# Kernel optimization log

Measured on AMD Instinct MI355X. Metric: run time of the kernel, lower is better.

Reference implementation:

```python
import jax, jax.numpy as jnp
import numpy as np

DIM = 512
HEADS = 8
EPS = 1e-5


def layer_norm(x, g, b):
    mu = jnp.mean(x, axis=-1, keepdims=True)
    var = jnp.mean(jnp.square(x - mu), axis=-1, keepdims=True)
    return (x - mu) * jax.lax.rsqrt(var + EPS) * g + b


def setup_inputs() -> dict:
    key = jax.random.key(0)
    ks = jax.random.split(key, 8)
    d = DIM
    s = 0.02
    return {
        "x": jax.random.normal(ks[0], (2, d, 64, 64), jnp.float32),
        "ln1_g": jnp.ones((d,), jnp.float32),
        "ln1_b": jnp.zeros((d,), jnp.float32),
        "w_qkv": jax.random.normal(ks[1], (d, 3 * d), jnp.float32) * s,
        "b_qkv": jnp.zeros((3 * d,), jnp.float32),
        "w_proj": jax.random.normal(ks[2], (d, d), jnp.float32) * s,
        "b_proj": jnp.zeros((d,), jnp.float32),
        "ln2_g": jnp.ones((d,), jnp.float32),
        "ln2_b": jnp.zeros((d,), jnp.float32),
        "w_ffn1": jax.random.normal(ks[3], (d, 4 * d), jnp.float32) * s,
        "b_ffn1": jnp.zeros((4 * d,), jnp.float32),
        "w_ffn2": jax.random.normal(ks[4], (4 * d, d), jnp.float32) * s,
        "b_ffn2": jnp.zeros((d,), jnp.float32),
    }


def reference(x, ln1_g, ln1_b, w_qkv, b_qkv, w_proj, b_proj,
              ln2_g, ln2_b, w_ffn1, b_ffn1, w_ffn2, b_ffn2):
    B, C, H, W = x.shape
    hd = C // HEADS
    x_in = x
    t = x.reshape(B, C, H * W).transpose(0, 2, 1)  # [B, N, C]
    h = layer_norm(t, ln1_g, ln1_b)
    qkv = h @ w_qkv + b_qkv  # [B, N, 3C]
    q, k, v = jnp.split(qkv, 3, axis=-1)
    def to_heads(a):
        return a.reshape(B, -1, HEADS, hd).transpose(0, 2, 1, 3)  # [B, h, N, hd]
    q, k, v = to_heads(q), to_heads(k), to_heads(v)
    # NOTE: module scales by 1/sqrt(C), not 1/sqrt(head_dim)
    attn = jnp.einsum('bhqd,bhkd->bhqk', q, k) / jnp.sqrt(jnp.float32(C))
    attn = jax.nn.softmax(attn, axis=-1)
    out = jnp.einsum('bhqk,bhkd->bhqd', attn, v)
    out = out.transpose(0, 2, 1, 3).reshape(B, -1, C)
    out = out @ w_proj + b_proj
    t = t + out
    h2 = layer_norm(t, ln2_g, ln2_b)
    ffn = jax.nn.relu(h2 @ w_ffn1 + b_ffn1) @ w_ffn2 + b_ffn2
    t = t + ffn
    y = t.transpose(0, 2, 1).reshape(B, C, H, W)
    return y + x_in
```

## Files before the change

kernel.cpp:

```cpp
#include <hip/hip_runtime.h>
#include <hip/hip_bf16.h>

typedef __bf16 bf16;
typedef __bf16 bf16x8 __attribute__((ext_vector_type(8)));
typedef __bf16 bf16x4 __attribute__((ext_vector_type(4)));
typedef __bf16 bf16x2 __attribute__((ext_vector_type(2)));
typedef float f32x4 __attribute__((ext_vector_type(4)));
typedef int int4v __attribute__((ext_vector_type(4)));
typedef int int2v __attribute__((ext_vector_type(2)));

#define DEV static __device__ __forceinline__

DEV void gload16(const void* g, void* l) {
    __builtin_amdgcn_global_load_lds(
        (const __attribute__((address_space(1))) void*)g,
        (__attribute__((address_space(3))) void*)l, 16, 0, 0);
}

DEV f32x4 mfma16(bf16x8 a, bf16x8 b, f32x4 c) {
    return __builtin_amdgcn_mfma_f32_16x16x32_bf16(a, b, c, 0, 0, 0);
}

DEV int cvtpk(float lo, float hi) {
    int r;
    asm("v_cvt_pk_bf16_f32 %0, %1, %2" : "=v"(r) : "v"(lo), "v"(hi));
    return r;
}

DEV float rexp2(float x) {
    float r;
    asm("v_exp_f32 %0, %1" : "=v"(r) : "v"(x));
    return r;
}

template <bool HASPO>
__global__ __launch_bounds__(512, 2)
void k_tln(const float* __restrict__ x, const bf16* __restrict__ po,
           const float* __restrict__ gg, const float* __restrict__ bb,
           bf16* __restrict__ h) {
    __shared__ char sm[HASPO ? 69632 : 35840];
    bf16* big = (bf16*)sm;
    float* red = (float*)(sm + 33536);
    float* mures = (float*)(sm + 35584);
    bf16* pob = (bf16*)(sm + 35840);

    int t = threadIdx.x;
    int bid = blockIdx.x;
    int nt = bid & 127, b = bid >> 7;
    int n0 = nt * 32;

    if (HASPO) {
        int rr = t >> 4, cs16 = t & 15;
        const bf16* ps = po + (size_t)(b * 4096 + n0 + rr) * 512 + cs16 * 32;
#pragma unroll
        for (int j = 0; j < 4; j++)
            *(bf16x8*)&pob[rr * 524 + cs16 * 32 + j * 8] =
                *(const bf16x8*)(ps + j * 8);
        __syncthreads();
    }

    int n = t & 31, cg = t >> 5;
    const float* xp = x + (size_t)b * 512 * 4096 +
                      (size_t)(cg * 32) * 4096 + n0 + n;
    float s = 0.f, ss = 0.f;
#pragma unroll
    for (int i = 0; i < 32; i++) {
        float v = xp[(size_t)i * 4096];
        if (HASPO) v += (float)pob[n * 524 + cg * 32 + i];
        s += v;
        ss += v * v;
        big[n * 524 + cg * 32 + i] = (bf16)v;
    }
    s += __shfl_xor(s, 32);
    ss += __shfl_xor(ss, 32);
    int w = t >> 6, l = t & 63;
    if (l < 32) {
        red[(w * 32 + n) * 2] = s;
        red[(w * 32 + n) * 2 + 1] = ss;
    }
    __syncthreads();
    if (t < 32) {
        float ts = 0.f, tss = 0.f;
#pragma unroll
        for (int ww = 0; ww < 8; ww++) {
            ts += red[(ww * 32 + t) * 2];
            tss += red[(ww * 32 + t) * 2 + 1];
        }
        float mu = ts * (1.f / 512.f);
        float var = tss * (1.f / 512.f) - mu * mu;
        mures[t * 2] = mu;
        mures[t * 2 + 1] = rsqrtf(var + 1e-5f);
    }
    __syncthreads();

    int nw = t >> 4, cs = t & 15;
    float mu = mures[nw * 2], rs = mures[nw * 2 + 1];
    bf16* hd = h + (size_t)(b * 4096 + n0 + nw) * 512;
#pragma unroll
    for (int j = 0; j < 4; j++) {
        int c = cs * 8 + j * 128;
        bf16x8 vv = *(const bf16x8*)&big[nw * 524 + c];
        f32x4 g0v = *(const f32x4*)(gg + c);
        f32x4 g1v = *(const f32x4*)(gg + c + 4);
        f32x4 b0v = *(const f32x4*)(bb + c);
        f32x4 b1v = *(const f32x4*)(bb + c + 4);
        bf16x8 o;
#pragma unroll
        for (int k = 0; k < 4; k++) {
            o[k] = (bf16)(((float)vv[k] - mu) * rs * g0v[k] + b0v[k]);
            o[k + 4] = (bf16)(((float)vv[k + 4] - mu) * rs * g1v[k] + b1v[k]);
        }
        *(bf16x8*)(hd + c) = o;
    }
}

__global__ __launch_bounds__(256)
void k_fin(const float* __restrict__ x, const bf16* __restrict__ po,
           const bf16* __restrict__ f2o, float* __restrict__ y) {
    __shared__ float ts[64][33];
    int bid = blockIdx.x;
    int nt = bid & 127, ct = (bid >> 7) & 7, b = bid >> 10;
    int n0 = nt * 32, c0 = ct * 64;
    int tid = threadIdx.x;
    int pi = tid & 31, nr = tid >> 5;
#pragma unroll
    for (int p = 0; p < 4; p++) {
        int n = nr + p * 8;
        size_t ro = (size_t)(b * 4096 + n0 + n) * 512 + c0 + pi * 2;
        bf16x2 pv = *(const bf16x2*)(po + ro);
        bf16x2 fv = *(const bf16x2*)(f2o + ro);
        ts[pi * 2][n] = (float)pv[0] + (float)fv[0];
        ts[pi * 2 + 1][n] = (float)pv[1] + (float)fv[1];
    }
    __syncthreads();
    int nw = tid & 31, cw = tid >> 5;
#pragma unroll
    for (int q = 0; q < 8; q++) {
        int c = cw + q * 8;
        size_t off = ((size_t)b * 512 + c0 + c) * 4096 + n0 + nw;
        y[off] = 2.0f * x[off] + ts[c][nw];
    }
}

__global__ __launch_bounds__(256)
void k_wtall(const float* __restrict__ w0, const float* __restrict__ w1,
             const float* __restrict__ w2, const float* __restrict__ w3,
             bf16* __restrict__ d0, bf16* __restrict__ d1,
             bf16* __restrict__ d2, bf16* __restrict__ d3) {
    __shared__ float tile[32][33];
    int bid = blockIdx.x;
    const float* w;
    bf16* d;
    int K, N, t;
    if (bid < 768)       { w = w0; d = d0; K = 512;  N = 1536; t = bid; }
    else if (bid < 1024) { w = w1; d = d1; K = 512;  N = 512;  t = bid - 768; }
    else if (bid < 2048) { w = w2; d = d2; K = 512;  N = 2048; t = bid - 1024; }
    else                 { w = w3; d = d3; K = 2048; N = 512;  t = bid - 2048; }
    int ntn = N >> 5;
    int kt = t / ntn, ntile = t % ntn;
    int k0 = kt * 32, n0 = ntile * 32;
    int tid = threadIdx.x;
    int nl = tid & 31, kl = tid >> 5;
#pragma unroll
    for (int i = 0; i < 4; i++) {
        int k = kl + i * 8;
        tile[k][nl] = w[(size_t)(k0 + k) * N + n0 + nl];
    }
    __syncthreads();
    int kl2 = tid & 31, nl2 = tid >> 5;
#pragma unroll
    for (int i = 0; i < 4; i++) {
        int n = nl2 + i * 8;
        d[(size_t)(n0 + n) * K + k0 + kl2] = (bf16)tile[kl2][n];
    }
}

template <int MODE, int BN>
__global__ __launch_bounds__(256, BN == 64 ? 3 : 2)
void k_gemm(const bf16* __restrict__ A, const bf16* __restrict__ BT,
            const float* __restrict__ bias, bf16* __restrict__ outb,
            bf16* __restrict__ vtout, int M, int N, int K) {
    constexpr int CG = BN / 32;
    constexpr int BSZ = CG * 4096;
    __shared__ char smem[32768 + 2 * BSZ];
    int ntn = N / BN;
    int nwg = gridDim.x;
    int bid = blockIdx.x;
    int cpx = nwg >> 3;
    bid = (bid & 7) * cpx + (bid >> 3);
    int bm = bid / ntn, bn = bid % ntn;
    int m0 = bm * 128, n0 = bn * BN;
    int tid = threadIdx.x;
    int w = tid >> 6, l = tid & 63;
    int wm = w >> 1, wn = w & 1;
    int l15 = l & 15, lg = l >> 4;

    f32x4 acc[4][CG];
#pragma unroll
    for (int i = 0; i < 4; i++)
#pragma unroll
        for (int j = 0; j < CG; j++) acc[i][j] = (f32x4){0.f, 0.f, 0.f, 0.f};

    int srow = tid >> 3, sphys = tid & 7;
    int lrow_a = wm * 64 + l15;
    int lrow_b = wn * (BN / 2) + l15;

#define GEMM_STAGE(k0v, bb)                                                  \
    do {                                                                     \
        _Pragma("unroll") for (int s = 0; s < 4; s++) {                      \
            int row = s * 32 + srow;                                         \
            int k16 = sphys ^ (row & 7);                                     \
            gload16(A + (size_t)(m0 + row) * K + (k0v) + k16 * 8,            \
                    smem + (bb) * 16384 + s * 4096 + tid * 16);              \
        }                                                                    \
        _Pragma("unroll") for (int s = 0; s < CG; s++) {                     \
            int row = s * 32 + srow;                                         \
            int k16 = sphys ^ (row & 7);                                     \
            gload16(BT + (size_t)(n0 + row) * K + (k0v) + k16 * 8,           \
                    smem + 32768 + (bb) * BSZ + s * 4096 + tid * 16);        \
        }                                                                    \
    } while (0)

    int nk = K >> 6;
    GEMM_STAGE(0, 0);
    int cur = 0;
    for (int kt = 0; kt < nk; kt++) {
        if (kt + 1 < nk) {
            GEMM_STAGE((kt + 1) << 6, cur ^ 1);
            if constexpr (BN == 128)
                asm volatile("s_waitcnt vmcnt(8)" ::: "memory");
            else
                asm volatile("s_waitcnt vmcnt(6)" ::: "memory");
        } else {
            asm volatile("s_waitcnt vmcnt(0)" ::: "memory");
        }
        __builtin_amdgcn_s_barrier();
        __builtin_amdgcn_sched_barrier(0);
        const char* pA = smem + cur * 16384;
        const char* pB = smem + 32768 + cur * BSZ;
#pragma unroll
        for (int ks = 0; ks < 2; ks++) {
            bf16x8 af[4], bfr[CG];
#pragma unroll
            for (int rg = 0; rg < 4; rg++) {
                int row = lrow_a + rg * 16;
                af[rg] = *(const bf16x8*)(pA + row * 128 +
                                          (((lg + ks * 4) ^ (row & 7)) << 4));
            }
#pragma unroll
            for (int cg = 0; cg < CG; cg++) {
                int row = lrow_b + cg * 16;
                bfr[cg] = *(const bf16x8*)(pB + row * 128 +
                                           (((lg + ks * 4) ^ (row & 7)) << 4));
            }
#pragma unroll
            for (int rg = 0; rg < 4; rg++)
#pragma unroll
                for (int cg = 0; cg < CG; cg++)
                    acc[rg][cg] = mfma16(af[rg], bfr[cg], acc[rg][cg]);
        }
        __builtin_amdgcn_s_barrier();
        cur ^= 1;
    }
#undef GEMM_STAGE

    if constexpr (MODE == 2) {
        if (n0 >= 1024) {
            char* vl = smem;
#pragma unroll
            for (int cg = 0; cg < CG; cg++) {
                int col = wn * (BN / 2) + cg * 16 + l15;
                float bz = bias[n0 + col];
#pragma unroll
                for (int rg = 0; rg < 4; rg++) {
                    int rowb = wm * 64 + rg * 16 + lg * 4;
                    int2v qq = {cvtpk(acc[rg][cg][0] + bz, acc[rg][cg][1] + bz),
                                cvtpk(acc[rg][cg][2] + bz, acc[rg][cg][3] + bz)};
                    *(int2v*)(vl + col * 272 + rowb * 2) = qq;
                }
            }
            __syncthreads();
            int b = m0 >> 12, nrow0 = m0 & 4095;
            int dl = tid >> 3, c8 = tid & 7;
#pragma unroll
            for (int dd = 0; dd < BN / 32; dd++) {
                int d = dd * 32 + dl;
                int ch = (n0 - 1024) + d;
                bf16* dst = vtout +
                    ((size_t)((b * 8 + (ch >> 6)) * 64 + (ch & 63))) * 4096 + nrow0;
#pragma unroll
                for (int half = 0; half < 2; half++) {
                    int chunk = half * 8 + c8;
                    bf16x8 vv = *(const bf16x8*)(vl + d * 272 + chunk * 16);
                    *(bf16x8*)(dst + chunk * 8) = vv;
                }
            }
            return;
        }
    }

    constexpr int RS = BN * 2 + 8;
    constexpr int CH = BN / 8;
    char* ep = smem;
#pragma unroll
    for (int cg = 0; cg < CG; cg++) {
        int lcol = wn * (BN / 2) + cg * 16 + l15;
        float bz = bias[n0 + lcol];
#pragma unroll
        for (int rg = 0; rg < 4; rg++) {
#pragma unroll
            for (int j = 0; j < 4; j++) {
                int lrow = wm * 64 + rg * 16 + lg * 4 + j;
                float v = acc[rg][cg][j] + bz;
                if (MODE == 1) v = fmaxf(v, 0.f);
                *(bf16*)(ep + lrow * RS + lcol * 2) = (bf16)v;
            }
        }
    }
    __syncthreads();
    int cch = tid & (CH - 1);
    int rof = tid / CH;
    constexpr int RPP = 256 / CH;
#pragma unroll
    for (int i = 0; i < 128 / RPP; i++) {
        int row = i * RPP + rof;
        bf16x8 vv = *(const bf16x8*)(ep + row * RS + cch * 16);
        *(bf16x8*)(outb + (size_t)(m0 + row) * N + n0 + cch * 8) = vv;
    }
}

__global__ __launch_bounds__(256, 4)
void k_attn(const bf16* __restrict__ qkvb, const bf16* __restrict__ vt,
            bf16* __restrict__ attno) {
    __shared__ bf16 sK[2][64 * 64];
    __shared__ bf16 sV[2][64 * 64];
    const float sc = 0.044194173824159216f * 1.4426950408889634f;
    int bid = blockIdx.x;
    int nb = (bid & 7) * 128 + (bid >> 3);
    int bh = nb >> 6, qt = nb & 63;
    int b = bh >> 3, hh = bh & 7;
    int q0 = qt * 64;
    int tid = threadIdx.x, w = tid >> 6, l = tid & 63;
    int l15 = l & 15, lg = l >> 4, l7 = l15 & 7;
    int lg4 = lg * 4;
    int vperm = ((lg & 1) << 1) | (lg >> 1);
    const bf16* qbase = qkvb + (size_t)b * 4096 * 1536 + hh * 64;
    const bf16* kbase = qbase + 512;
    const bf16* vbase = vt + (size_t)bh * 64 * 4096;
    int srow = tid >> 3, sphys = tid & 7;

    const char* kp0 = (const char*)&sK[0][0] + l15 * 128 + ((lg ^ l7) << 4);
    const char* kp1 = (const char*)&sK[0][0] + l15 * 128 + (((4 + lg) ^ l7) << 4);
    const char* vp0 = (const char*)&sV[0][0] + l15 * 128 + ((vperm ^ l7) << 4);
    const char* vp1 = (const char*)&sV[0][0] + l15 * 128 + (((4 + vperm) ^ l7) << 4);
    char* dK0 = (char*)&sK[0][0] + tid * 16;
    char* dV0 = (char*)&sV[0][0] + tid * 16;
    const char* kg = (const char*)(kbase + srow * 1536 + (sphys ^ (srow & 7)) * 8);
    const char* vg = (const char*)(vbase + srow * 4096 + (sphys ^ (srow & 7)) * 8);

    gload16(kg, dK0);
    gload16(kg + 98304, dK0 + 4096);
    gload16(vg, dV0);
    gload16(vg + 262144, dV0 + 4096);
    kg += 196608;
    vg += 128;

    bf16x8 qf[2];
#pragma unroll
    for (int ks = 0; ks < 2; ks++) {
        bf16x8 v = *(const bf16x8*)(qbase +
            (size_t)(q0 + w * 16 + l15) * 1536 + ks * 32 + lg * 8);
        bf16x8 o;
#pragma unroll
        for (int j = 0; j < 8; j++) o[j] = (bf16)((float)v[j] * sc);
        qf[ks] = o;
    }

    const f32x4 kZ = {0.f, 0.f, 0.f, 0.f};
    float lsum = 0.f;
    f32x4 acc[4];
#pragma unroll
    for (int df = 0; df < 4; df++) acc[df] = kZ;

#define ABODY(BUF, PF)                                                        \
    {                                                                         \
        if (PF) {                                                             \
            gload16(kg, dK0 + (1 - (BUF)) * 8192);                            \
            gload16(kg + 98304, dK0 + (1 - (BUF)) * 8192 + 4096);             \
            gload16(vg, dV0 + (1 - (BUF)) * 8192);                            \
            gload16(vg + 262144, dV0 + (1 - (BUF)) * 8192 + 4096);            \
            kg += 196608;                                                     \
            vg += 128;                                                        \
            asm volatile("s_waitcnt vmcnt(4)" ::: "memory");                  \
        } else {                                                              \
            asm volatile("s_waitcnt vmcnt(0)" ::: "memory");                  \
        }                                                                     \
        __builtin_amdgcn_s_barrier();                                         \
        __builtin_amdgcn_sched_barrier(0);                                    \
        f32x4 s0, s1, s2, s3;                                                 \
        __builtin_amdgcn_s_setprio(1);                                        \
        s0 = mfma16(*(const bf16x8*)(kp0 + (BUF) * 8192 + 0 * 2048), qf[0], kZ); \
        s0 = mfma16(*(const bf16x8*)(kp1 + (BUF) * 8192 + 0 * 2048), qf[1], s0); \
        s1 = mfma16(*(const bf16x8*)(kp0 + (BUF) * 8192 + 1 * 2048), qf[0], kZ); \
        s1 = mfma16(*(const bf16x8*)(kp1 + (BUF) * 8192 + 1 * 2048), qf[1], s1); \
        __builtin_amdgcn_s_setprio(0);                                        \
        float e0 = rexp2(s0[0]), e1 = rexp2(s0[1]);                           \
        float e2 = rexp2(s0[2]), e3 = rexp2(s0[3]);                           \
        float e4 = rexp2(s1[0]), e5 = rexp2(s1[1]);                           \
        float e6 = rexp2(s1[2]), e7 = rexp2(s1[3]);                           \
        __builtin_amdgcn_s_setprio(1);                                        \
        s2 = mfma16(*(const bf16x8*)(kp0 + (BUF) * 8192 + 2 * 2048), qf[0], kZ); \
        s2 = mfma16(*(const bf16x8*)(kp1 + (BUF) * 8192 + 2 * 2048), qf[1], s2); \
        s3 = mfma16(*(const bf16x8*)(kp0 + (BUF) * 8192 + 3 * 2048), qf[0], kZ); \
        s3 = mfma16(*(const bf16x8*)(kp1 + (BUF) * 8192 + 3 * 2048), qf[1], s3); \
        __builtin_amdgcn_s_setprio(0);                                        \
        int p0 = cvtpk(e0, e1), p1 = cvtpk(e2, e3);                           \
        int p2 = cvtpk(e4, e5), p3 = cvtpk(e6, e7);                           \
        asm("v_permlane16_swap_b32 %0, %1" : "+v"(p2), "+v"(p0));             \
        asm("v_permlane16_swap_b32 %0, %1" : "+v"(p3), "+v"(p1));             \
        {                                                                     \
            int4v ai = {p0, p1, p2, p3};                                      \
            bf16x8 af = __builtin_bit_cast(bf16x8, ai);                       \
            __builtin_amdgcn_s_setprio(1);                                    \
            acc[0] = mfma16(af, *(const bf16x8*)(vp0 + (BUF) * 8192 + 0 * 2048), acc[0]); \
            acc[1] = mfma16(af, *(const bf16x8*)(vp0 + (BUF) * 8192 + 1 * 2048), acc[1]); \
            acc[2] = mfma16(af, *(const bf16x8*)(vp0 + (BUF) * 8192 + 2 * 2048), acc[2]); \
            acc[3] = mfma16(af, *(const bf16x8*)(vp0 + (BUF) * 8192 + 3 * 2048), acc[3]); \
            __builtin_amdgcn_s_setprio(0);                                    \
        }                                                                     \
        float e8 = rexp2(s2[0]), e9 = rexp2(s2[1]);                           \
        float e10 = rexp2(s2[2]), e11 = rexp2(s2[3]);                         \
        float e12 = rexp2(s3[0]), e13 = rexp2(s3[1]);                         \
        float e14 = rexp2(s3[2]), e15 = rexp2(s3[3]);                         \
        int p4 = cvtpk(e8, e9), p5 = cvtpk(e10, e11);                         \
        int p6 = cvtpk(e12, e13), p7 = cvtpk(e14, e15);                       \
        asm("v_permlane16_swap_b32 %0, %1" : "+v"(p6), "+v"(p4));             \
        asm("v_permlane16_swap_b32 %0, %1" : "+v"(p7), "+v"(p5));             \
        {                                                                     \
            int4v ai = {p4, p5, p6, p7};                                      \
            bf16x8 af = __builtin_bit_cast(bf16x8, ai);                       \
            __builtin_amdgcn_s_setprio(1);                                    \
            acc[0] = mfma16(af, *(const bf16x8*)(vp1 + (BUF) * 8192 + 0 * 2048), acc[0]); \
            acc[1] = mfma16(af, *(const bf16x8*)(vp1 + (BUF) * 8192 + 1 * 2048), acc[1]); \
            acc[2] = mfma16(af, *(const bf16x8*)(vp1 + (BUF) * 8192 + 2 * 2048), acc[2]); \
            acc[3] = mfma16(af, *(const bf16x8*)(vp1 + (BUF) * 8192 + 3 * 2048), acc[3]); \
            __builtin_amdgcn_s_setprio(0);                                    \
        }                                                                     \
        lsum += (((e0 + e1) + (e2 + e3)) + ((e4 + e5) + (e6 + e7))) +         \
                (((e8 + e9) + (e10 + e11)) + ((e12 + e13) + (e14 + e15)));    \
        __builtin_amdgcn_s_barrier();                                         \
    }

    for (int tt = 0; tt < 31; tt++) {
        ABODY(0, 1)
        ABODY(1, 1)
    }
    ABODY(0, 1)
    ABODY(1, 0)
#undef ABODY

    lsum += __shfl_xor(lsum, 16);
    lsum += __shfl_xor(lsum, 32);
    float invq[4];
#pragma unroll
    for (int j = 0; j < 4; j++)
        invq[j] = 1.0f / __shfl(lsum, lg4 + j);

    bf16* ow = (bf16*)&sK[0][0] + w * 16 * 64;
#pragma unroll
    for (int df = 0; df < 4; df++) {
        int chunk = df * 2 + (l15 >> 3);
        int within = l15 & 7;
#pragma unroll
        for (int j = 0; j < 4; j++) {
            int q = lg * 4 + j;
            *(bf16*)((char*)ow + q * 128 + ((chunk ^ (q & 7)) << 4) + within * 2) =
                (bf16)(acc[df][j] * invq[j]);
        }
    }
    __syncthreads();
    const char* owr = (const char*)ow;
#pragma unroll
    for (int half = 0; half < 2; half++) {
        int r = l >> 2, ch = (l & 3) + half * 4;
        bf16x8 vv = *(const bf16x8*)(owr + r * 128 + ((ch ^ (r & 7)) << 4));
        *(bf16x8*)(attno + (size_t)(b * 4096 + q0 + w * 16 + r) * 512 +
                   hh * 64 + ch * 8) = vv;
    }
}

extern "C" void kernel_launch(void* const* d_in, const int* in_sizes, int n_in,
                              void* d_out, int out_size, void* d_ws, size_t ws_size,
                              hipStream_t stream) {
    const float* x = (const float*)d_in[0];
    const float* ln1g = (const float*)d_in[1];
    const float* ln1b = (const float*)d_in[2];
    const float* wqkv = (const float*)d_in[3];
    const float* bqkv = (const float*)d_in[4];
    const float* wproj = (const float*)d_in[5];
    const float* bproj = (const float*)d_in[6];
    const float* ln2g = (const float*)d_in[7];
    const float* ln2b = (const float*)d_in[8];
    const float* wffn1 = (const float*)d_in[9];
    const float* bffn1 = (const float*)d_in[10];
    const float* wffn2 = (const float*)d_in[11];
    const float* bffn2 = (const float*)d_in[12];
    float* y = (float*)d_out;

    char* ws = (char*)d_ws;
    bf16* po   = (bf16*)(ws + 0);
    bf16* f2o  = (bf16*)(ws + 8388608);
    bf16* h    = (bf16*)(ws + 16777216);
    bf16* qkvb = (bf16*)(ws + 25165824);
    bf16* vtb  = (bf16*)(ws + 50331648);
    bf16* f1   = (bf16*)(ws + 25165824);
    bf16* wqT  = (bf16*)(ws + 58720256);
    bf16* wpT  = (bf16*)(ws + 60293120);
    bf16* w1T  = (bf16*)(ws + 60817408);
    bf16* w2T  = (bf16*)(ws + 62914560);
    bf16* attno = h;

    k_tln<false><<<256, 512, 0, stream>>>(x, nullptr, ln1g, ln1b, h);
    k_wtall<<<3072, 256, 0, stream>>>(wqkv, wproj, wffn1, wffn2,
                                      wqT, wpT, w1T, w2T);
    k_gemm<2, 128><<<768, 256, 0, stream>>>(h, wqT, bqkv, qkvb, vtb,
                                            8192, 1536, 512);
    k_attn<<<1024, 256, 0, stream>>>(qkvb, vtb, attno);
    k_gemm<0, 64><<<512, 256, 0, stream>>>(attno, wpT, bproj, po, nullptr,
                                           8192, 512, 512);
    k_tln<true><<<256, 512, 0, stream>>>(x, po, ln2g, ln2b, h);
    k_gemm<1, 128><<<1024, 256, 0, stream>>>(h, w1T, bffn1, f1, nullptr,
                                             8192, 2048, 512);
    k_gemm<0, 64><<<512, 256, 0, stream>>>(f1, w2T, bffn2, f2o, nullptr,
                                           8192, 512, 2048);
    k_fin<<<2048, 256, 0, stream>>>(x, po, f2o, y);
}
```

Measured before the change: 188.6 us.

## Fuse final residual/transpose into FFN2 GEMM epilogue; compute softmax row sums via MFMA

Adds a MODE 3 epilogue to the GEMM that adds bias and the projection output, transposes through shared memory, and writes y = 2x + t directly in NCHW layout. This removes the separate finalize kernel and the f2o intermediate round trip through global memory. Separately, the attention kernel now accumulates softmax row sums with an extra MFMA against a vector of ones instead of scalar adds and cross-lane shuffles. That moves VALU work onto the matrix unit but sums bf16-rounded probabilities, and the epilogue reads po with scattered scalar bf16 loads.

```diff
diff --git a/kernel.cpp b/kernel.cpp
--- a/kernel.cpp
+++ b/kernel.cpp
@@ -111,34 +111,6 @@
             o[k + 4] = (bf16)(((float)vv[k + 4] - mu) * rs * g1v[k] + b1v[k]);
         }
         *(bf16x8*)(hd + c) = o;
-    }
-}
-
-__global__ __launch_bounds__(256)
-void k_fin(const float* __restrict__ x, const bf16* __restrict__ po,
-           const bf16* __restrict__ f2o, float* __restrict__ y) {
-    __shared__ float ts[64][33];
-    int bid = blockIdx.x;
-    int nt = bid & 127, ct = (bid >> 7) & 7, b = bid >> 10;
-    int n0 = nt * 32, c0 = ct * 64;
-    int tid = threadIdx.x;
-    int pi = tid & 31, nr = tid >> 5;
-#pragma unroll
-    for (int p = 0; p < 4; p++) {
-        int n = nr + p * 8;
-        size_t ro = (size_t)(b * 4096 + n0 + n) * 512 + c0 + pi * 2;
-        bf16x2 pv = *(const bf16x2*)(po + ro);
-        bf16x2 fv = *(const bf16x2*)(f2o + ro);
-        ts[pi * 2][n] = (float)pv[0] + (float)fv[0];
-        ts[pi * 2 + 1][n] = (float)pv[1] + (float)fv[1];
-    }
-    __syncthreads();
-    int nw = tid & 31, cw = tid >> 5;
-#pragma unroll
-    for (int q = 0; q < 8; q++) {
-        int c = cw + q * 8;
-        size_t off = ((size_t)b * 512 + c0 + c) * 4096 + n0 + nw;
-        y[off] = 2.0f * x[off] + ts[c][nw];
     }
 }
 
@@ -179,7 +151,9 @@
 __global__ __launch_bounds__(256, BN == 64 ? 3 : 2)
 void k_gemm(const bf16* __restrict__ A, const bf16* __restrict__ BT,
             const float* __restrict__ bias, bf16* __restrict__ outb,
-            bf16* __restrict__ vtout, int M, int N, int K) {
+            bf16* __restrict__ vtout, const float* __restrict__ xin,
+            const bf16* __restrict__ poin, float* __restrict__ yout,
+            int M, int N, int K) {
     constexpr int CG = BN / 32;
     constexpr int BSZ = CG * 4096;
     __shared__ char smem[32768 + 2 * BSZ];
@@ -299,6 +273,40 @@
         }
     }
 
+    if constexpr (MODE == 3) {
+        float* ts = (float*)smem;
+        int b = m0 >> 12, nrow0 = m0 & 4095;
+#pragma unroll
+        for (int cg = 0; cg < CG; cg++) {
+            int lcol = wn * (BN / 2) + cg * 16 + l15;
+            float bz = bias[n0 + lcol];
+#pragma unroll
+            for (int rg = 0; rg < 4; rg++) {
+#pragma unroll
+                for (int j = 0; j < 4; j++) {
+                    int lrow = wm * 64 + rg * 16 + lg * 4 + j;
+                    float v = acc[rg][cg][j] + bz +
+                        (float)poin[(size_t)(m0 + lrow) * 512 + n0 + lcol];
+                    ts[lcol * 132 + lrow] = v;
+                }
+            }
+        }
+        __syncthreads();
+        int nl = (tid & 31) * 4, chh = tid >> 5;
+#pragma unroll
+        for (int q = 0; q < 8; q++) {
+            int c = chh + q * 8;
+            size_t off = ((size_t)b * 512 + n0 + c) * 4096 + nrow0 + nl;
+            f32x4 xv = *(const f32x4*)(xin + off);
+            f32x4 tv = *(const f32x4*)&ts[c * 132 + nl];
+            f32x4 ov;
+#pragma unroll
+            for (int k2 = 0; k2 < 4; k2++) ov[k2] = 2.f * xv[k2] + tv[k2];
+            *(f32x4*)(yout + off) = ov;
+        }
+        return;
+    }
+
     constexpr int RS = BN * 2 + 8;
     constexpr int CH = BN / 8;
     char* ep = smem;
@@ -342,7 +350,6 @@
     int q0 = qt * 64;
     int tid = threadIdx.x, w = tid >> 6, l = tid & 63;
     int l15 = l & 15, lg = l >> 4, l7 = l15 & 7;
-    int lg4 = lg * 4;
     int vperm = ((lg & 1) << 1) | (lg >> 1);
     const bf16* qbase = qkvb + (size_t)b * 4096 * 1536 + hh * 64;
     const bf16* kbase = qbase + 512;
@@ -375,9 +382,12 @@
         for (int j = 0; j < 8; j++) o[j] = (bf16)((float)v[j] * sc);
         qf[ks] = o;
     }
+    bf16x8 ones;
+#pragma unroll
+    for (int j = 0; j < 8; j++) ones[j] = (bf16)1.0f;
 
     const f32x4 kZ = {0.f, 0.f, 0.f, 0.f};
-    float lsum = 0.f;
+    f32x4 accl = kZ;
     f32x4 acc[4];
 #pragma unroll
     for (int df = 0; df < 4; df++) acc[df] = kZ;
@@ -426,6 +436,7 @@
             acc[1] = mfma16(af, *(const bf16x8*)(vp0 + (BUF) * 8192 + 1 * 2048), acc[1]); \
             acc[2] = mfma16(af, *(const bf16x8*)(vp0 + (BUF) * 8192 + 2 * 2048), acc[2]); \
             acc[3] = mfma16(af, *(const bf16x8*)(vp0 + (BUF) * 8192 + 3 * 2048), acc[3]); \
+            accl = mfma16(af, ones, accl);                                    \
             __builtin_amdgcn_s_setprio(0);                                    \
         }                                                                     \
         float e8 = rexp2(s2[0]), e9 = rexp2(s2[1]);                           \
@@ -444,10 +455,9 @@
             acc[1] = mfma16(af, *(const bf16x8*)(vp1 + (BUF) * 8192 + 1 * 2048), acc[1]); \
             acc[2] = mfma16(af, *(const bf16x8*)(vp1 + (BUF) * 8192 + 2 * 2048), acc[2]); \
             acc[3] = mfma16(af, *(const bf16x8*)(vp1 + (BUF) * 8192 + 3 * 2048), acc[3]); \
+            accl = mfma16(af, ones, accl);                                    \
             __builtin_amdgcn_s_setprio(0);                                    \
         }                                                                     \
-        lsum += (((e0 + e1) + (e2 + e3)) + ((e4 + e5) + (e6 + e7))) +         \
-                (((e8 + e9) + (e10 + e11)) + ((e12 + e13) + (e14 + e15)));    \
         __builtin_amdgcn_s_barrier();                                         \
     }
 
@@ -459,12 +469,9 @@
     ABODY(1, 0)
 #undef ABODY
 
-    lsum += __shfl_xor(lsum, 16);
-    lsum += __shfl_xor(lsum, 32);
     float invq[4];
 #pragma unroll
-    for (int j = 0; j < 4; j++)
-        invq[j] = 1.0f / __shfl(lsum, lg4 + j);
+    for (int j = 0; j < 4; j++) invq[j] = 1.0f / accl[j];
 
     bf16* ow = (bf16*)&sK[0][0] + w * 16 * 64;
 #pragma unroll
@@ -509,7 +516,6 @@
 
     char* ws = (char*)d_ws;
     bf16* po   = (bf16*)(ws + 0);
-    bf16* f2o  = (bf16*)(ws + 8388608);
     bf16* h    = (bf16*)(ws + 16777216);
     bf16* qkvb = (bf16*)(ws + 25165824);
     bf16* vtb  = (bf16*)(ws + 50331648);
@@ -524,14 +530,16 @@
     k_wtall<<<3072, 256, 0, stream>>>(wqkv, wproj, wffn1, wffn2,
                                       wqT, wpT, w1T, w2T);
     k_gemm<2, 128><<<768, 256, 0, stream>>>(h, wqT, bqkv, qkvb, vtb,
+                                            nullptr, nullptr, nullptr,
                                             8192, 1536, 512);
     k_attn<<<1024, 256, 0, stream>>>(qkvb, vtb, attno);
     k_gemm<0, 64><<<512, 256, 0, stream>>>(attno, wpT, bproj, po, nullptr,
+                                           nullptr, nullptr, nullptr,
                                            8192, 512, 512);
     k_tln<true><<<256, 512, 0, stream>>>(x, po, ln2g, ln2b, h);
     k_gemm<1, 128><<<1024, 256, 0, stream>>>(h, w1T, bffn1, f1, nullptr,
+                                             nullptr, nullptr, nullptr,
                                              8192, 2048, 512);
-    k_gemm<0, 64><<<512, 256, 0, stream>>>(f1, w2T, bffn2, f2o, nullptr,
-                                           8192, 512, 2048);
-    k_fin<<<2048, 256, 0, stream>>>(x, po, f2o, y);
-}
+    k_gemm<3, 64><<<512, 256, 0, stream>>>(f1, w2T, bffn2, nullptr, nullptr,
+                                           x, po, y, 8192, 512, 2048);
+}
```

Result: faster. 181.0 us (-4.0%).
